# Kernel tuning notes

Measured on AMD Instinct MI355X. Metric: run time of the kernel, lower is better.

## Reference

```python
import jax, jax.numpy as jnp
import numpy as np

N_NODES = 100000
N_EDGES = 3200000
D_IN = 128
D_OUT = 128


def setup_inputs() -> dict:
    key = jax.random.key(0)
    k1, k2, k3, k4, k5, k6 = jax.random.split(key, 6)
    x = jax.random.normal(k1, (N_NODES, D_IN), dtype=jnp.float32)
    edge_val = jax.random.uniform(k2, (N_EDGES,), dtype=jnp.float32)
    weight = jax.random.normal(k3, (D_IN, D_OUT), dtype=jnp.float32) / np.sqrt(D_IN)
    bias = jax.random.normal(k4, (D_OUT,), dtype=jnp.float32) * 0.01
    edge_row = jax.random.randint(k5, (N_EDGES,), 0, N_NODES, dtype=jnp.int64)
    edge_col = jax.random.randint(k6, (N_EDGES,), 0, N_NODES, dtype=jnp.int64)
    return {"x": x, "edge_val": edge_val, "weight": weight, "bias": bias,
            "edge_row": edge_row, "edge_col": edge_col}


def reference(x, edge_val, weight, bias, edge_row, edge_col):
    # support = Linear(x): [N, D_out]
    support = jnp.einsum("ni,io->no", x, weight) + bias
    # output = spmm(adj, support): gather source-node features, weight by
    # edge value, scatter-add into destination rows.
    msgs = edge_val[:, None] * support[edge_col]  # [E, D_out]
    output = jax.ops.segment_sum(msgs, edge_row, num_segments=N_NODES)
    return output
```

## Files before the change

### kernel.cpp

```cpp
#include <hip/hip_runtime.h>

#define N_NODES 100000
#define N_EDGES 3200000
#define D 128

#define BSPAN 64
#define NB 1563
#define CAP 2560
#define PBLOCKS 256
#define PCHUNK (N_EDGES / PBLOCKS)
#define OVF_CAP 8192

#define SUP_OFF     0ULL
#define RECS_OFF    25600000ULL
#define TAILS_OFF   (RECS_OFF + (size_t)NB * CAP * 8)
#define OVFCNT_OFF  (TAILS_OFF + (size_t)NB * 4)
#define OVF_OFF     ((OVFCNT_OFF + 15) & ~15ULL)
#define WS_NEED     (OVF_OFF + (size_t)OVF_CAP * 12)

typedef short short8 __attribute__((ext_vector_type(8)));
typedef float floatx4 __attribute__((ext_vector_type(4)));
typedef unsigned short ushort8v __attribute__((ext_vector_type(8)));

__device__ inline ushort f2bf(float f) {
  uint u = __float_as_uint(f);
  u += 0x7FFF + ((u >> 16) & 1);
  return (ushort)(u >> 16);
}
__device__ inline float bf_lo(uint b) { return __uint_as_float(b << 16); }
__device__ inline float bf_hi(uint b) { return __uint_as_float(b & 0xFFFF0000u); }

#define LSTR 136

__global__ __launch_bounds__(256) void gcn_gemm_mfma(
    const float* __restrict__ x, const float* __restrict__ W,
    const float* __restrict__ bias, ushort* __restrict__ support, int M) {
  __shared__ ushort WT[D * LSTR];
  __shared__ ushort XT[BSPAN * LSTR];

  const int t = threadIdx.x;
  const int w = t >> 6;
  const int lane = t & 63;
  const int quad = lane >> 4;
  const int l16 = lane & 15;
  const int row0 = blockIdx.x * BSPAN;

  for (int i = t * 4; i < D * D; i += 1024) {
    const int k = i >> 7, n = i & 127;
    const float4 wv = *(const float4*)&W[i];
    WT[(n + 0) * LSTR + k] = f2bf(wv.x);
    WT[(n + 1) * LSTR + k] = f2bf(wv.y);
    WT[(n + 2) * LSTR + k] = f2bf(wv.z);
    WT[(n + 3) * LSTR + k] = f2bf(wv.w);
  }
  for (int i = t * 4; i < BSPAN * D; i += 1024) {
    const int m = i >> 7, k = i & 127;
    const int r = row0 + m;
    float4 xv = make_float4(0.f, 0.f, 0.f, 0.f);
    if (r < M) xv = *(const float4*)&x[(size_t)r * D + k];
    ushort4 pv;
    pv.x = f2bf(xv.x); pv.y = f2bf(xv.y); pv.z = f2bf(xv.z); pv.w = f2bf(xv.w);
    *(ushort4*)&XT[m * LSTR + k] = pv;
  }
  __syncthreads();

  floatx4 acc[8];
#pragma unroll
  for (int nt = 0; nt < 8; nt++) acc[nt] = (floatx4)0.f;

#pragma unroll
  for (int kc = 0; kc < 4; kc++) {
    const short8 a = *(const short8*)&XT[(w * 16 + l16) * LSTR + kc * 32 + quad * 8];
#pragma unroll
    for (int nt = 0; nt < 8; nt++) {
      const short8 b = *(const short8*)&WT[(nt * 16 + l16) * LSTR + kc * 32 + quad * 8];
      acc[nt] = __builtin_amdgcn_mfma_f32_16x16x32_bf16(a, b, acc[nt], 0, 0, 0);
    }
  }

  float bs[8];
#pragma unroll
  for (int nt = 0; nt < 8; nt++) bs[nt] = bias[nt * 16 + l16];

  __syncthreads();
#pragma unroll
  for (int nt = 0; nt < 8; nt++)
#pragma unroll
    for (int r = 0; r < 4; r++)
      XT[(w * 16 + quad * 4 + r) * LSTR + nt * 16 + l16] = f2bf(acc[nt][r] + bs[nt]);
  __syncthreads();

  for (int i = t * 8; i < BSPAN * D; i += 2048) {
    const int m = i >> 7, k = i & 127;
    const int r = row0 + m;
    if (r < M)
      *(ushort8v*)&support[(size_t)r * D + k] = *(const ushort8v*)&XT[m * LSTR + k];
  }
}

__global__ __launch_bounds__(1024) void partition_kernel(
    const int* __restrict__ erow, const int* __restrict__ ecol,
    const float* __restrict__ eval, int* __restrict__ tails,
    int2* __restrict__ recs, int* __restrict__ ovf_cnt,
    int3* __restrict__ ovf) {
  __shared__ int cnt[NB];
  __shared__ int cursor[NB];
  const int t = threadIdx.x;
  for (int i = t; i < NB; i += 1024) cnt[i] = 0;
  __syncthreads();

  const int e0 = blockIdx.x * PCHUNK;
  for (int e = e0 + t; e < e0 + PCHUNK; e += 1024)
    atomicAdd(&cnt[erow[e] >> 6], 1);
  __syncthreads();

  for (int i = t; i < NB; i += 1024) {
    const int c = cnt[i];
    cursor[i] = (c > 0) ? atomicAdd(&tails[i], c) : 0;
  }
  __syncthreads();

  for (int e = e0 + t; e < e0 + PCHUNK; e += 1024) {
    const int row = erow[e];
    const int b = row >> 6;
    const int pos = atomicAdd(&cursor[b], 1);
    const int col = ecol[e];
    const int vb = __float_as_int(eval[e]);
    if (pos < CAP) {
      recs[(size_t)b * CAP + pos] = make_int2(col | ((row & 63) << 20), vb);
    } else {
      const int oi = atomicAdd(ovf_cnt, 1);
      if (oi < OVF_CAP) ovf[oi] = make_int3(row, col, vb);
    }
  }
}

__global__ __launch_bounds__(256) void bucket_gather(
    const ushort* __restrict__ sup, const int* __restrict__ tails,
    const int2* __restrict__ recs, float* __restrict__ out) {
  __shared__ int2 lrec[CAP];
  __shared__ int rcnt[BSPAN];
  __shared__ int rstart[BSPAN];
  __shared__ int rend[BSPAN];
  __shared__ int rpos[BSPAN];

  const int bi = blockIdx.x;
  const int t = threadIdx.x;
  const int n = min(tails[bi], CAP);
  const int2* __restrict__ gbase = recs + (size_t)bi * CAP;

  if (t < BSPAN) rcnt[t] = 0;
  __syncthreads();

  int2 rcache[10];
  int nr = 0;
  for (int i = t; i < n; i += 256) rcache[nr++] = gbase[i];

  for (int j = 0; j < nr; j++) atomicAdd(&rcnt[rcache[j].x >> 20], 1);
  __syncthreads();

  if (t < 64) {
    const int c = rcnt[t];
    int v = c;
#pragma unroll
    for (int off = 1; off < 64; off <<= 1) {
      const int u = __shfl_up(v, off);
      if (t >= off) v += u;
    }
    rend[t] = v;
    rstart[t] = v - c;
    rpos[t] = v - c;
  }
  __syncthreads();

  for (int j = 0; j < nr; j++) {
    const int2 rc = rcache[j];
    const int p = atomicAdd(&rpos[rc.x >> 20], 1);
    lrec[p] = make_int2((rc.x & 0xFFFFF) << 8, rc.y);
  }
  __syncthreads();

  const int lane = t & 63;
  const int w = t >> 6;
  const int h = lane >> 5;
  const int hl = lane & 31;
  const char* __restrict__ supb = (const char*)sup;

  for (int j = 0; j < 16; j++) {
    const int rr = w * 16 + j;
    const int s = rstart[rr];
    const int e = rend[rr];
    float4 acc = make_float4(0.f, 0.f, 0.f, 0.f);
#pragma unroll 2
    for (int i = s; i < e; i += 2) {
      const int idx = i + h;
      const int2 rc = lrec[min(idx, CAP - 1)];
      const bool valid = idx < e;
      const int coff = valid ? rc.x : 0;
      const float val = valid ? __int_as_float(rc.y) : 0.f;
      const uint2 b = *(const uint2*)(supb + coff + hl * 8);
      acc.x += val * bf_lo(b.x);
      acc.y += val * bf_hi(b.x);
      acc.z += val * bf_lo(b.y);
      acc.w += val * bf_hi(b.y);
    }
    acc.x += __shfl_xor(acc.x, 32);
    acc.y += __shfl_xor(acc.y, 32);
    acc.z += __shfl_xor(acc.z, 32);
    acc.w += __shfl_xor(acc.w, 32);
    const int row = bi * BSPAN + rr;
    if (h == 0 && row < N_NODES)
      *(float4*)&out[(size_t)row * D + hl * 4] = acc;
  }
}

__global__ __launch_bounds__(256) void ovf_apply(
    const int* __restrict__ ovf_cnt, const int3* __restrict__ ovf,
    const ushort* __restrict__ sup, float* __restrict__ out) {
  const int tid = blockIdx.x * 256 + threadIdx.x;
  const int e = tid >> 5;
  const int n = min(*ovf_cnt, OVF_CAP);
  if (e >= n) return;
  const int3 rec = ovf[e];
  const float val = __int_as_float(rec.z);
  const int j = (tid & 31) * 4;
#pragma unroll
  for (int k = 0; k < 4; k++) {
    const float f = __uint_as_float(((uint)sup[(size_t)rec.y * D + j + k]) << 16);
    unsafeAtomicAdd(&out[(size_t)rec.x * D + j + k], val * f);
  }
}

__global__ __launch_bounds__(256) void gcn_spmm_atomic(
    const ushort* __restrict__ sup, const float* __restrict__ edge_val,
    const int* __restrict__ edge_row, const int* __restrict__ edge_col,
    float* __restrict__ out) {
  const long long tid = (long long)blockIdx.x * blockDim.x + threadIdx.x;
  const int e = (int)(tid >> 5);
  if (e >= N_EDGES) return;
  const int j = ((int)tid & 31) * 4;
  const int col = edge_col[e];
  const int row = edge_row[e];
  const float val = edge_val[e];
#pragma unroll
  for (int k = 0; k < 4; k++) {
    const float f = __uint_as_float(((uint)sup[(size_t)col * D + j + k]) << 16);
    unsafeAtomicAdd(&out[(size_t)row * D + j + k], val * f);
  }
}

extern "C" void kernel_launch(void* const* d_in, const int* in_sizes, int n_in,
                              void* d_out, int out_size, void* d_ws,
                              size_t ws_size, hipStream_t stream) {
  const float* x        = (const float*)d_in[0];
  const float* edge_val = (const float*)d_in[1];
  const float* W        = (const float*)d_in[2];
  const float* bias     = (const float*)d_in[3];
  const int*   edge_row = (const int*)d_in[4];
  const int*   edge_col = (const int*)d_in[5];
  float* out = (float*)d_out;

  char* ws = (char*)d_ws;
  ushort* support = (ushort*)(ws + SUP_OFF);

  const int gemm_blocks = (N_NODES + BSPAN - 1) / BSPAN;
  gcn_gemm_mfma<<<gemm_blocks, 256, 0, stream>>>(x, W, bias, support, N_NODES);

  if (ws_size >= WS_NEED) {
    int2* recs   = (int2*)(ws + RECS_OFF);
    int*  tails  = (int*)(ws + TAILS_OFF);
    int*  ovfcnt = (int*)(ws + OVFCNT_OFF);
    int3* ovf    = (int3*)(ws + OVF_OFF);

    hipMemsetAsync(tails, 0, (size_t)NB * 4 + 4, stream);
    partition_kernel<<<PBLOCKS, 1024, 0, stream>>>(edge_row, edge_col, edge_val,
                                                   tails, recs, ovfcnt, ovf);
    bucket_gather<<<NB, 256, 0, stream>>>(support, tails, recs, out);
    ovf_apply<<<OVF_CAP * 32 / 256, 256, 0, stream>>>(ovfcnt, ovf, support, out);
  } else {
    hipMemsetAsync(out, 0, (size_t)out_size * sizeof(float), stream);
    const long long spmm_threads = (long long)N_EDGES * 32;
    gcn_spmm_atomic<<<(int)((spmm_threads + 255) / 256), 256, 0, stream>>>(
        support, edge_val, edge_row, edge_col, out);
  }
}
```

Measured before the change: 354.8 us.

## Halve gather bucket span and widen per-lane support loads to 16 bytes

The row bucket size drops from 64 to 32 rows, which doubles the number of buckets and halves the per-bucket capacity and shared-memory footprint. The GEMM tile is decoupled into its own MT constant so it keeps 64 rows. In the gather, each row's neighbors are processed four at a time by 16-lane groups, each loading 16 bytes (8 bf16) per lane instead of 8 bytes, followed by a two-step shuffle reduction. A launch-bounds occupancy hint of 8 blocks per SM is added. The intent is to raise memory-level parallelism and occupancy in the gather. The costs are more partition buckets, more atomics on tails, and a possibly higher overflow rate with the smaller per-bucket cap (mean 1024 edges against a cap of 1280).

```diff
diff --git a/kernel.cpp b/kernel.cpp
--- a/kernel.cpp
+++ b/kernel.cpp
@@ -4,9 +4,10 @@
 #define N_EDGES 3200000
 #define D 128
 
-#define BSPAN 64
-#define NB 1563
-#define CAP 2560
+#define MT 64
+#define BSPAN 32
+#define NB 3125
+#define CAP 1280
 #define PBLOCKS 256
 #define PCHUNK (N_EDGES / PBLOCKS)
 #define OVF_CAP 8192
@@ -36,14 +37,14 @@
     const float* __restrict__ x, const float* __restrict__ W,
     const float* __restrict__ bias, ushort* __restrict__ support, int M) {
   __shared__ ushort WT[D * LSTR];
-  __shared__ ushort XT[BSPAN * LSTR];
+  __shared__ ushort XT[MT * LSTR];
 
   const int t = threadIdx.x;
   const int w = t >> 6;
   const int lane = t & 63;
   const int quad = lane >> 4;
   const int l16 = lane & 15;
-  const int row0 = blockIdx.x * BSPAN;
+  const int row0 = blockIdx.x * MT;
 
   for (int i = t * 4; i < D * D; i += 1024) {
     const int k = i >> 7, n = i & 127;
@@ -53,7 +54,7 @@
     WT[(n + 2) * LSTR + k] = f2bf(wv.z);
     WT[(n + 3) * LSTR + k] = f2bf(wv.w);
   }
-  for (int i = t * 4; i < BSPAN * D; i += 1024) {
+  for (int i = t * 4; i < MT * D; i += 1024) {
     const int m = i >> 7, k = i & 127;
     const int r = row0 + m;
     float4 xv = make_float4(0.f, 0.f, 0.f, 0.f);
@@ -90,7 +91,7 @@
       XT[(w * 16 + quad * 4 + r) * LSTR + nt * 16 + l16] = f2bf(acc[nt][r] + bs[nt]);
   __syncthreads();
 
-  for (int i = t * 8; i < BSPAN * D; i += 2048) {
+  for (int i = t * 8; i < MT * D; i += 2048) {
     const int m = i >> 7, k = i & 127;
     const int r = row0 + m;
     if (r < M)
@@ -111,7 +112,7 @@
 
   const int e0 = blockIdx.x * PCHUNK;
   for (int e = e0 + t; e < e0 + PCHUNK; e += 1024)
-    atomicAdd(&cnt[erow[e] >> 6], 1);
+    atomicAdd(&cnt[erow[e] >> 5], 1);
   __syncthreads();
 
   for (int i = t; i < NB; i += 1024) {
@@ -122,12 +123,12 @@
 
   for (int e = e0 + t; e < e0 + PCHUNK; e += 1024) {
     const int row = erow[e];
-    const int b = row >> 6;
+    const int b = row >> 5;
     const int pos = atomicAdd(&cursor[b], 1);
     const int col = ecol[e];
     const int vb = __float_as_int(eval[e]);
     if (pos < CAP) {
-      recs[(size_t)b * CAP + pos] = make_int2(col | ((row & 63) << 20), vb);
+      recs[(size_t)b * CAP + pos] = make_int2(col | ((row & 31) << 20), vb);
     } else {
       const int oi = atomicAdd(ovf_cnt, 1);
       if (oi < OVF_CAP) ovf[oi] = make_int3(row, col, vb);
@@ -135,7 +136,7 @@
   }
 }
 
-__global__ __launch_bounds__(256) void bucket_gather(
+__global__ __launch_bounds__(256, 8) void bucket_gather(
     const ushort* __restrict__ sup, const int* __restrict__ tails,
     const int2* __restrict__ recs, float* __restrict__ out) {
   __shared__ int2 lrec[CAP];
@@ -152,18 +153,18 @@
   if (t < BSPAN) rcnt[t] = 0;
   __syncthreads();
 
-  int2 rcache[10];
+  int2 rcache[5];
   int nr = 0;
   for (int i = t; i < n; i += 256) rcache[nr++] = gbase[i];
 
   for (int j = 0; j < nr; j++) atomicAdd(&rcnt[rcache[j].x >> 20], 1);
   __syncthreads();
 
-  if (t < 64) {
+  if (t < BSPAN) {
     const int c = rcnt[t];
     int v = c;
 #pragma unroll
-    for (int off = 1; off < 64; off <<= 1) {
+    for (int off = 1; off < BSPAN; off <<= 1) {
       const int u = __shfl_up(v, off);
       if (t >= off) v += u;
     }
@@ -182,35 +183,49 @@
 
   const int lane = t & 63;
   const int w = t >> 6;
-  const int h = lane >> 5;
-  const int hl = lane & 31;
+  const int g = lane >> 4;
+  const int gl = lane & 15;
   const char* __restrict__ supb = (const char*)sup;
 
-  for (int j = 0; j < 16; j++) {
-    const int rr = w * 16 + j;
+  for (int j = 0; j < 8; j++) {
+    const int rr = w * 8 + j;
     const int s = rstart[rr];
     const int e = rend[rr];
-    float4 acc = make_float4(0.f, 0.f, 0.f, 0.f);
+    float4 acc0 = make_float4(0.f, 0.f, 0.f, 0.f);
+    float4 acc1 = make_float4(0.f, 0.f, 0.f, 0.f);
 #pragma unroll 2
-    for (int i = s; i < e; i += 2) {
-      const int idx = i + h;
+    for (int i = s; i < e; i += 4) {
+      const int idx = i + g;
       const int2 rc = lrec[min(idx, CAP - 1)];
       const bool valid = idx < e;
       const int coff = valid ? rc.x : 0;
       const float val = valid ? __int_as_float(rc.y) : 0.f;
-      const uint2 b = *(const uint2*)(supb + coff + hl * 8);
-      acc.x += val * bf_lo(b.x);
-      acc.y += val * bf_hi(b.x);
-      acc.z += val * bf_lo(b.y);
-      acc.w += val * bf_hi(b.y);
-    }
-    acc.x += __shfl_xor(acc.x, 32);
-    acc.y += __shfl_xor(acc.y, 32);
-    acc.z += __shfl_xor(acc.z, 32);
-    acc.w += __shfl_xor(acc.w, 32);
+      const uint4 b = *(const uint4*)(supb + coff + gl * 16);
+      acc0.x += val * bf_lo(b.x);
+      acc0.y += val * bf_hi(b.x);
+      acc0.z += val * bf_lo(b.y);
+      acc0.w += val * bf_hi(b.y);
+      acc1.x += val * bf_lo(b.z);
+      acc1.y += val * bf_hi(b.z);
+      acc1.z += val * bf_lo(b.w);
+      acc1.w += val * bf_hi(b.w);
+    }
+#pragma unroll
+    for (int off = 16; off <= 32; off <<= 1) {
+      acc0.x += __shfl_xor(acc0.x, off);
+      acc0.y += __shfl_xor(acc0.y, off);
+      acc0.z += __shfl_xor(acc0.z, off);
+      acc0.w += __shfl_xor(acc0.w, off);
+      acc1.x += __shfl_xor(acc1.x, off);
+      acc1.y += __shfl_xor(acc1.y, off);
+      acc1.z += __shfl_xor(acc1.z, off);
+      acc1.w += __shfl_xor(acc1.w, off);
+    }
     const int row = bi * BSPAN + rr;
-    if (h == 0 && row < N_NODES)
-      *(float4*)&out[(size_t)row * D + hl * 4] = acc;
+    if (g == 0 && row < N_NODES) {
+      *(float4*)&out[(size_t)row * D + gl * 8] = acc0;
+      *(float4*)&out[(size_t)row * D + gl * 8 + 4] = acc1;
+    }
   }
 }
 
@@ -263,7 +278,7 @@
   char* ws = (char*)d_ws;
   ushort* support = (ushort*)(ws + SUP_OFF);
 
-  const int gemm_blocks = (N_NODES + BSPAN - 1) / BSPAN;
+  const int gemm_blocks = (N_NODES + MT - 1) / MT;
   gcn_gemm_mfma<<<gemm_blocks, 256, 0, stream>>>(x, W, bias, support, N_NODES);
 
   if (ws_size >= WS_NEED) {
```

New measurement: 360.9 us. Within noise of the previous version (+1.7%).
